# Kernel tuning notes

Measured on AMD Instinct MI355X. Metric: run time of the kernel, lower is better.

## Reference

```python
import jax, jax.numpy as jnp
import numpy as np

N = 50000

def gcn_conv(x, W, b, src, dst, n_nodes):
    # PyG GCNConv: h = x @ W; add self-loops; sym-normalize; scatter-add; + bias
    h = x @ W  # [N, d_out]
    loop = jnp.arange(n_nodes, dtype=src.dtype)
    s = jnp.concatenate([src, loop])
    d = jnp.concatenate([dst, loop])
    deg = jax.ops.segment_sum(jnp.ones_like(d, dtype=h.dtype), d, num_segments=n_nodes)
    dinv = jnp.where(deg > 0, jax.lax.rsqrt(deg), 0.0)
    norm = dinv[s] * dinv[d]  # [E+N]
    msgs = h[s] * norm[:, None]  # gather + scale
    out = jax.ops.segment_sum(msgs, d, num_segments=n_nodes)  # scatter-add
    return out + b

def setup_inputs() -> dict:
    key = jax.random.key(0)
    k1, k2, k3, k4 = jax.random.split(key, 4)
    in_c, hid_c, out_c, E = 512, 256, 64, 800000
    x = jax.random.normal(k1, (N, in_c), dtype=jnp.float32)
    edge_index = jax.random.randint(k2, (2, E), 0, N, dtype=jnp.int64)
    W1 = jax.random.normal(k3, (in_c, hid_c), dtype=jnp.float32) / np.sqrt(in_c)
    b1 = jnp.zeros((hid_c,), dtype=jnp.float32)
    W2 = jax.random.normal(k4, (hid_c, out_c), dtype=jnp.float32) / np.sqrt(hid_c)
    b2 = jnp.zeros((out_c,), dtype=jnp.float32)
    return {"x": x, "edge_index": edge_index, "W1": W1, "b1": b1, "W2": W2, "b2": b2}

def reference(x, edge_index, W1, b1, W2, b2):
    src, dst = edge_index[0], edge_index[1]
    h = gcn_conv(x, W1, b1, src, dst, N)
    h = jax.nn.relu(h)
    h = gcn_conv(h, W2, b2, src, dst, N)
    return jax.nn.log_softmax(h, axis=1)
```

## Files before the change

kernel.cpp:

```cpp
#include <hip/hip_runtime.h>
#include <hip/hip_bf16.h>

#define IN_C 512
#define HID_C 256
#define OUT_C 64

typedef __attribute__((ext_vector_type(8))) short bf16x8;
typedef __attribute__((ext_vector_type(4))) float f32x4;
typedef __attribute__((ext_vector_type(2))) float f32x2;

__device__ __forceinline__ ushort f2bf(float f) {
  __hip_bfloat16 h = __float2bfloat16(f);
  union { __hip_bfloat16 h; ushort u; } v; v.h = h; return v.u;
}
__device__ __forceinline__ uint pack2bf(float a, float b) {
  return (uint)f2bf(a) | ((uint)f2bf(b) << 16);
}
__device__ __forceinline__ float u2f(uint u) {
  union { uint i; float f; } v; v.i = u; return v.f;
}
__device__ __forceinline__ void pkacc(f32x2& aLo, f32x2& aHi, uint ux, uint uy) {
  f32x2 lo, hi;
  lo[0] = u2f(ux << 16);         lo[1] = u2f(uy << 16);
  hi[0] = u2f(ux & 0xffff0000u); hi[1] = u2f(uy & 0xffff0000u);
  aLo += lo;
  aHi += hi;
}
__device__ __forceinline__ void glds16(const ushort* g, ushort* l) {
  __builtin_amdgcn_global_load_lds(
      (const __attribute__((address_space(1))) unsigned int*)(const void*)g,
      (__attribute__((address_space(3))) unsigned int*)(void*)l, 16, 0, 0);
}


__global__ void deg_count(const int* __restrict__ dst, int* __restrict__ counts, int E) {
  int e = blockIdx.x * 256 + threadIdx.x;
  if (e >= E) return;
  atomicAdd(&counts[dst[e]], 1);
}

#define SCAN_TILE 1024

__global__ __launch_bounds__(256) void scan_block_sums(const int* __restrict__ counts,
                                                       int* __restrict__ partial, int n) {
  int base = blockIdx.x * SCAN_TILE + threadIdx.x * 4;
  int s = 0;
  if (base + 3 < n) {
    int4 v = *(const int4*)(counts + base);
    s = v.x + v.y + v.z + v.w;
  } else {
#pragma unroll
    for (int i = 0; i < 4; ++i) if (base + i < n) s += counts[base + i];
  }
#pragma unroll
  for (int off = 1; off < 64; off <<= 1) s += __shfl_xor(s, off);
  __shared__ int ws[4];
  int lane = threadIdx.x & 63, wid = threadIdx.x >> 6;
  if (lane == 0) ws[wid] = s;
  __syncthreads();
  if (threadIdx.x == 0) partial[blockIdx.x] = ws[0] + ws[1] + ws[2] + ws[3];
}

__global__ void scan_partials(int* __restrict__ partial, int nb) {
  int lane = threadIdx.x;
  int carry = 0;
  for (int base = 0; base < nb; base += 64) {
    int i = base + lane;
    int v = (i < nb) ? partial[i] : 0;
    int incl = v;
#pragma unroll
    for (int off = 1; off < 64; off <<= 1) {
      int y = __shfl_up(incl, off);
      if (lane >= off) incl += y;
    }
    if (i < nb) partial[i] = carry + incl - v;
    carry += __shfl(incl, 63);
  }
}

__global__ __launch_bounds__(256) void scan_write(const int* __restrict__ counts,
                                                  const int* __restrict__ partial,
                                                  int* __restrict__ offs,
                                                  int* __restrict__ cur,
                                                  float* __restrict__ dinv,
                                                  int n, int E) {
  int tid = threadIdx.x;
  int base = blockIdx.x * SCAN_TILE + tid * 4;
  int4 c = make_int4(0, 0, 0, 0);
  if (base + 3 < n) {
    c = *(const int4*)(counts + base);
  } else {
    if (base + 0 < n) c.x = counts[base + 0];
    if (base + 1 < n) c.y = counts[base + 1];
    if (base + 2 < n) c.z = counts[base + 2];
  }
  int tsum = c.x + c.y + c.z + c.w;
  int lane = tid & 63, wid = tid >> 6;
  int incl = tsum;
#pragma unroll
  for (int off = 1; off < 64; off <<= 1) {
    int y = __shfl_up(incl, off);
    if (lane >= off) incl += y;
  }
  __shared__ int ws[4];
  if (lane == 63) ws[wid] = incl;
  __syncthreads();
  int wbase = 0;
#pragma unroll
  for (int w = 0; w < 4; ++w) if (w < wid) wbase += ws[w];
  int off0 = partial[blockIdx.x] + wbase + (incl - tsum);
  int4 ov;
  ov.x = off0;
  ov.y = off0 + c.x;
  ov.z = off0 + c.x + c.y;
  ov.w = off0 + c.x + c.y + c.z;
  float4 dv;
  dv.x = rsqrtf((float)(c.x + 1));
  dv.y = rsqrtf((float)(c.y + 1));
  dv.z = rsqrtf((float)(c.z + 1));
  dv.w = rsqrtf((float)(c.w + 1));
  if (base + 3 < n) {
    *(int4*)(offs + base) = ov;
    *(int4*)(cur + base) = ov;
    *(float4*)(dinv + base) = dv;
  } else {
    int o4[4] = {ov.x, ov.y, ov.z, ov.w};
    float d4[4] = {dv.x, dv.y, dv.z, dv.w};
    for (int i = 0; i < 4; ++i)
      if (base + i < n) { offs[base + i] = o4[i]; cur[base + i] = o4[i]; dinv[base + i] = d4[i]; }
  }
  if (blockIdx.x == 0 && tid == 0) offs[n] = E;
}

__global__ void fill_adj(const int* __restrict__ src, const int* __restrict__ dst,
                         int* __restrict__ cur, int* __restrict__ adj, int E) {
  int e = blockIdx.x * 256 + threadIdx.x;
  if (e >= E) return;
  int pos = atomicAdd(&cur[dst[e]], 1);
  adj[pos] = src[e];
}

__global__ __launch_bounds__(256) void transpose_w2(const float* __restrict__ W1,
                                                    ushort* __restrict__ W1t,
                                                    const float* __restrict__ W2,
                                                    ushort* __restrict__ W2t) {
  const float* W; ushort* Wt; int K, N;
  if (blockIdx.z == 0) { W = W1; Wt = W1t; K = IN_C; N = HID_C; }
  else                 { W = W2; Wt = W2t; K = HID_C; N = OUT_C; }
  int n0 = blockIdx.x * 32;
  int k0 = blockIdx.y * 32;
  if (n0 >= N || k0 >= K) return;
  __shared__ ushort t[32][33];
  int tx = threadIdx.x & 31;
  int ty = threadIdx.x >> 5;
#pragma unroll
  for (int i = 0; i < 4; ++i) {
    int k = k0 + ty + i * 8;
    t[ty + i * 8][tx] = f2bf(W[(size_t)k * N + n0 + tx]);
  }
  __syncthreads();
#pragma unroll
  for (int i = 0; i < 4; ++i) {
    int n = n0 + ty + i * 8;
    Wt[(size_t)n * K + k0 + tx] = t[tx][ty + i * 8];
  }
}


__global__ __launch_bounds__(512) void gemm1_fs(const float* __restrict__ A,
                                                const ushort* __restrict__ Bt,
                                                const float* __restrict__ dinv,
                                                ushort* __restrict__ C, int M) {
  __shared__ __align__(16) ushort As[2][128 * 32];
  __shared__ __align__(16) ushort Bs[2][256 * 32];
  int tid = threadIdx.x;
  int lane = tid & 63, wid = tid >> 6;
  int m0 = blockIdx.x * 128;
  int arow = tid >> 2, acol = (tid & 3) * 8;
  int gma = m0 + arow; if (gma >= M) gma = M - 1;
  const float* gA = A + (size_t)gma * IN_C + acol;
  int rb0 = tid >> 2, cb0 = (tid & 3) * 8;
  int rb1 = (tid + 512) >> 2;
  const ushort* gB0 = Bt + (size_t)rb0 * IN_C + cb0;
  const ushort* gB1 = Bt + (size_t)rb1 * IN_C + cb0;

  int wr = wid >> 2, wc = wid & 3;
  int kf = (lane >> 4) * 8, rl = lane & 15;
  f32x4 acc[4][4] = {};

  {
    float4 p0 = *(const float4*)gA;
    float4 p1 = *(const float4*)(gA + 4);
    glds16(gB0, &Bs[0][tid * 8]);
    glds16(gB1, &Bs[0][(tid + 512) * 8]);
    uint4 w;
    w.x = pack2bf(p0.x, p0.y); w.y = pack2bf(p0.z, p0.w);
    w.z = pack2bf(p1.x, p1.y); w.w = pack2bf(p1.z, p1.w);
    *(uint4*)&As[0][arow * 32 + acol] = w;
  }
  __syncthreads();

  int cur = 0;
  for (int t = 0; t < 16; ++t) {
    float4 p0, p1;
    if (t < 15) {
      const float* g = gA + (t + 1) * 32;
      p0 = *(const float4*)g;
      p1 = *(const float4*)(g + 4);
      glds16(gB0 + (t + 1) * 32, &Bs[cur ^ 1][tid * 8]);
      glds16(gB1 + (t + 1) * 32, &Bs[cur ^ 1][(tid + 512) * 8]);
    }
    bf16x8 af[4], bf[4];
#pragma unroll
    for (int i = 0; i < 4; ++i)
      af[i] = *(const bf16x8*)&As[cur][(wr * 64 + i * 16 + rl) * 32 + kf];
#pragma unroll
    for (int j = 0; j < 4; ++j)
      bf[j] = *(const bf16x8*)&Bs[cur][(wc * 64 + j * 16 + rl) * 32 + kf];
#pragma unroll
    for (int i = 0; i < 4; ++i)
#pragma unroll
      for (int j = 0; j < 4; ++j)
        acc[i][j] = __builtin_amdgcn_mfma_f32_16x16x32_bf16(af[i], bf[j], acc[i][j], 0, 0, 0);
    if (t < 15) {
      uint4 w;
      w.x = pack2bf(p0.x, p0.y); w.y = pack2bf(p0.z, p0.w);
      w.z = pack2bf(p1.x, p1.y); w.w = pack2bf(p1.z, p1.w);
      *(uint4*)&As[cur ^ 1][arow * 32 + acol] = w;
    }
    __syncthreads();
    cur ^= 1;
  }

  int r4 = (lane >> 4) * 4;
  int cl = lane & 15;
#pragma unroll
  for (int i = 0; i < 4; ++i) {
#pragma unroll
    for (int r = 0; r < 4; ++r) {
      int gr = m0 + wr * 64 + i * 16 + r4 + r;
      if (gr < M) {
        float dv = dinv[gr];
#pragma unroll
        for (int j = 0; j < 4; ++j) {
          int gc = wc * 64 + j * 16 + cl;
          C[(size_t)gr * HID_C + gc] = f2bf(dv * acc[i][j][r]);
        }
      }
    }
  }
}

__global__ __launch_bounds__(256) void gemm2(const ushort* __restrict__ A,
                                             const ushort* __restrict__ Bt,
                                             const float* __restrict__ dinv,
                                             ushort* __restrict__ C, int M) {
  __shared__ __align__(16) ushort As[2][64 * 32];
  __shared__ __align__(16) ushort Bs[2][64 * 32];
  int tid = threadIdx.x;
  int lane = tid & 63, wid = tid >> 6;
  int m0 = blockIdx.x * 64;
  int arow = tid >> 2, acol = (tid & 3) * 8;
  int gma = m0 + arow; if (gma >= M) gma = M - 1;
  const ushort* gA = A + (size_t)gma * HID_C + acol;
  const ushort* gB = Bt + (size_t)arow * HID_C + acol;

  int wm = wid * 16;
  int kf = (lane >> 4) * 8, rl = lane & 15;
  f32x4 acc[4] = {};

  glds16(gA, &As[0][tid * 8]);
  glds16(gB, &Bs[0][tid * 8]);
  __syncthreads();

  int cur = 0;
  for (int t = 0; t < 8; ++t) {
    if (t < 7) {
      int k0 = (t + 1) * 32;
      glds16(gA + k0, &As[cur ^ 1][tid * 8]);
      glds16(gB + k0, &Bs[cur ^ 1][tid * 8]);
    }
    bf16x8 a, b[4];
    a = *(const bf16x8*)&As[cur][(wm + rl) * 32 + kf];
#pragma unroll
    for (int j = 0; j < 4; ++j)
      b[j] = *(const bf16x8*)&Bs[cur][(j * 16 + rl) * 32 + kf];
#pragma unroll
    for (int j = 0; j < 4; ++j)
      acc[j] = __builtin_amdgcn_mfma_f32_16x16x32_bf16(a, b[j], acc[j], 0, 0, 0);
    __syncthreads();
    cur ^= 1;
  }

  int r4 = (lane >> 4) * 4;
  int cl = lane & 15;
#pragma unroll
  for (int r = 0; r < 4; ++r) {
    int gr = m0 + wm + r4 + r;
    if (gr < M) {
      float dv = dinv[gr];
#pragma unroll
      for (int j = 0; j < 4; ++j) {
        int gc = j * 16 + cl;
        C[(size_t)gr * OUT_C + gc] = f2bf(dv * acc[j][r]);
      }
    }
  }
}


__global__ __launch_bounds__(256) void agg1(const ushort* __restrict__ h,
                                            ushort* __restrict__ out,
                                            const float* __restrict__ dinv,
                                            const int* __restrict__ offs,
                                            const int* __restrict__ adj,
                                            const float* __restrict__ bias, int Nn) {
  int node = blockIdx.x * 4 + (threadIdx.x >> 6);
  if (node >= Nn) return;
  int lane = threadIdx.x & 63;
  int slot = lane >> 4;
  int c0 = (lane & 15) * 16;
  int e0 = offs[node];
  int cnt = offs[node + 1] - e0 + 1;
  const ushort* hc = h + c0;
  f32x2 aLo[4] = {}, aHi[4] = {};
  for (int b0 = 0; b0 < cnt; b0 += 64) {
    int vk = b0 + lane;
    int myadj = node;
    if (vk > 0 && vk < cnt) myadj = adj[e0 + vk - 1];
    int bn = cnt - b0; if (bn > 64) bn = 64;
    int iters = (bn + 3) >> 2;
#pragma unroll 4
    for (int i = 0; i < iters; ++i) {
      int k = slot + 4 * i;
      int s = __shfl(myadj, k < bn ? k : 0);
      if (k < bn) {
        const uint4* rp = (const uint4*)(hc + (size_t)s * HID_C);
        uint4 u0 = rp[0];
        uint4 u1 = rp[1];
        pkacc(aLo[0], aHi[0], u0.x, u0.y);
        pkacc(aLo[1], aHi[1], u0.z, u0.w);
        pkacc(aLo[2], aHi[2], u1.x, u1.y);
        pkacc(aLo[3], aHi[3], u1.z, u1.w);
      }
    }
  }
  float r16[16];
#pragma unroll
  for (int q = 0; q < 4; ++q) {
    r16[4 * q + 0] = aLo[q][0];
    r16[4 * q + 1] = aHi[q][0];
    r16[4 * q + 2] = aLo[q][1];
    r16[4 * q + 3] = aHi[q][1];
  }
#pragma unroll
  for (int i = 0; i < 16; ++i) {
    r16[i] += __shfl_xor(r16[i], 16);
    r16[i] += __shfl_xor(r16[i], 32);
  }
  if (lane < 16) {
    float dv = dinv[node];
    const float4* bp = (const float4*)(bias + c0);
    float bb[16];
#pragma unroll
    for (int q = 0; q < 4; ++q) {
      float4 b4 = bp[q];
      bb[q * 4 + 0] = b4.x; bb[q * 4 + 1] = b4.y;
      bb[q * 4 + 2] = b4.z; bb[q * 4 + 3] = b4.w;
    }
    uint r[8];
#pragma unroll
    for (int i = 0; i < 8; ++i) {
      float v0 = fmaxf(dv * r16[2 * i]     + bb[2 * i],     0.f);
      float v1 = fmaxf(dv * r16[2 * i + 1] + bb[2 * i + 1], 0.f);
      r[i] = (uint)f2bf(v0) | ((uint)f2bf(v1) << 16);
    }
    uint4* op = (uint4*)(out + (size_t)node * HID_C + c0);
    op[0] = make_uint4(r[0], r[1], r[2], r[3]);
    op[1] = make_uint4(r[4], r[5], r[6], r[7]);
  }
}

__global__ __launch_bounds__(256) void agg2(const ushort* __restrict__ h,
                                            float* __restrict__ out,
                                            const float* __restrict__ dinv,
                                            const int* __restrict__ offs,
                                            const int* __restrict__ adj,
                                            const float* __restrict__ bias, int Nn) {
  int node = blockIdx.x * 4 + (threadIdx.x >> 6);
  if (node >= Nn) return;
  int lane = threadIdx.x & 63;
  int slot = lane >> 3;
  int c0 = (lane & 7) * 8;
  int e0 = offs[node];
  int cnt = offs[node + 1] - e0 + 1;
  const ushort* hc = h + c0;
  f32x2 aLo[2] = {}, aHi[2] = {};
  for (int b0 = 0; b0 < cnt; b0 += 64) {
    int vk = b0 + lane;
    int myadj = node;
    if (vk > 0 && vk < cnt) myadj = adj[e0 + vk - 1];
    int bn = cnt - b0; if (bn > 64) bn = 64;
    int iters = (bn + 7) >> 3;
#pragma unroll 4
    for (int i = 0; i < iters; ++i) {
      int k = slot + 8 * i;
      int s = __shfl(myadj, k < bn ? k : 0);
      if (k < bn) {
        uint4 u = *(const uint4*)(hc + (size_t)s * OUT_C);
        pkacc(aLo[0], aHi[0], u.x, u.y);
        pkacc(aLo[1], aHi[1], u.z, u.w);
      }
    }
  }
  float r8[8];
#pragma unroll
  for (int q = 0; q < 2; ++q) {
    r8[4 * q + 0] = aLo[q][0];
    r8[4 * q + 1] = aHi[q][0];
    r8[4 * q + 2] = aLo[q][1];
    r8[4 * q + 3] = aHi[q][1];
  }
#pragma unroll
  for (int i = 0; i < 8; ++i) {
    r8[i] += __shfl_xor(r8[i], 8);
    r8[i] += __shfl_xor(r8[i], 16);
    r8[i] += __shfl_xor(r8[i], 32);
  }
  float dv = dinv[node];
  const float4* bp = (const float4*)(bias + c0);
  float4 bb0 = bp[0], bb1 = bp[1];
  float v[8];
  v[0] = dv * r8[0] + bb0.x; v[1] = dv * r8[1] + bb0.y;
  v[2] = dv * r8[2] + bb0.z; v[3] = dv * r8[3] + bb0.w;
  v[4] = dv * r8[4] + bb1.x; v[5] = dv * r8[5] + bb1.y;
  v[6] = dv * r8[6] + bb1.z; v[7] = dv * r8[7] + bb1.w;
  float m = v[0];
#pragma unroll
  for (int i = 1; i < 8; ++i) m = fmaxf(m, v[i]);
  m = fmaxf(m, __shfl_xor(m, 1));
  m = fmaxf(m, __shfl_xor(m, 2));
  m = fmaxf(m, __shfl_xor(m, 4));
  float s8 = 0.f;
#pragma unroll
  for (int i = 0; i < 8; ++i) s8 += expf(v[i] - m);
  s8 += __shfl_xor(s8, 1);
  s8 += __shfl_xor(s8, 2);
  s8 += __shfl_xor(s8, 4);
  float lg = logf(s8);
  if (lane < 8) {
    float4* op = (float4*)(out + (size_t)node * OUT_C + c0);
    op[0] = make_float4(v[0] - m - lg, v[1] - m - lg, v[2] - m - lg, v[3] - m - lg);
    op[1] = make_float4(v[4] - m - lg, v[5] - m - lg, v[6] - m - lg, v[7] - m - lg);
  }
}


extern "C" void kernel_launch(void* const* d_in, const int* in_sizes, int n_in,
                              void* d_out, int out_size, void* d_ws, size_t ws_size,
                              hipStream_t stream) {
  const float* x  = (const float*)d_in[0];
  const int*   ei = (const int*)d_in[1];
  const float* W1 = (const float*)d_in[2];
  const float* b1 = (const float*)d_in[3];
  const float* W2 = (const float*)d_in[4];
  const float* b2 = (const float*)d_in[5];
  float* outp = (float*)d_out;

  int Nn = in_sizes[0] / IN_C;
  int E  = in_sizes[1] / 2;
  const int* srcv = ei;
  const int* dstv = ei + E;

  char* ws = (char*)d_ws;
  size_t o = 0;
  auto alloc = [&](size_t bytes) {
    char* p = ws + o;
    o = (o + bytes + 255) & ~(size_t)255;
    return p;
  };
  float*  dinv  = (float*)alloc((size_t)Nn * 4);
  int*    counts= (int*)alloc((size_t)Nn * 4);
  int*    offs  = (int*)alloc((size_t)(Nn + 1) * 4);
  int*    cur   = (int*)alloc((size_t)Nn * 4);
  int*    adj   = (int*)alloc((size_t)E * 4);
  int*    partial=(int*)alloc((size_t)((Nn + SCAN_TILE - 1) / SCAN_TILE) * 4);
  ushort* W1t   = (ushort*)alloc((size_t)IN_C * HID_C * 2);
  ushort* W2t   = (ushort*)alloc((size_t)HID_C * OUT_C * 2);
  ushort* h1p   = (ushort*)alloc((size_t)Nn * HID_C * 2);
  ushort* h1a   = (ushort*)alloc((size_t)Nn * HID_C * 2);
  ushort* h2p   = (ushort*)alloc((size_t)Nn * OUT_C * 2);

  int eb = (E + 255) / 256;
  int sb = (Nn + SCAN_TILE - 1) / SCAN_TILE;

  hipMemsetAsync(counts, 0, (size_t)Nn * 4, stream);
  deg_count<<<eb, 256, 0, stream>>>(dstv, counts, E);
  scan_block_sums<<<sb, 256, 0, stream>>>(counts, partial, Nn);
  scan_partials<<<1, 64, 0, stream>>>(partial, sb);
  scan_write<<<sb, 256, 0, stream>>>(counts, partial, offs, cur, dinv, Nn, E);
  fill_adj<<<eb, 256, 0, stream>>>(srcv, dstv, cur, adj, E);
  transpose_w2<<<dim3(HID_C / 32, IN_C / 32, 2), 256, 0, stream>>>(W1, W1t, W2, W2t);

  gemm1_fs<<<(Nn + 127) / 128, 512, 0, stream>>>(x, W1t, dinv, h1p, Nn);
  agg1<<<(Nn + 3) / 4, 256, 0, stream>>>(h1p, h1a, dinv, offs, adj, b1, Nn);
  gemm2<<<(Nn + 63) / 64, 256, 0, stream>>>(h1a, W2t, dinv, h2p, Nn);
  agg2<<<(Nn + 3) / 4, 256, 0, stream>>>(h2p, outp, dinv, offs, adj, b2, Nn);
}
```

Measured before the change: 231.2 us.

## Fuse weight transpose into degree count, inline partial scan, split GEMM1 over N

Merges the weight transpose into the degree-count launch as extra blocks, and drops the single-block partial-scan kernel by having each scan_write block reduce the preceding block partials itself. This removes two kernel launches and one serial tiny kernel. GEMM1 is retiled from 512-thread blocks covering all 256 output columns to 256-thread blocks covering 128 columns, with a second grid dimension. That doubles the block count, but each x row tile is now read and converted twice. The inline scan assumes no more than 64 scan tiles.

```diff
diff --git a/kernel.cpp b/kernel.cpp
--- a/kernel.cpp
+++ b/kernel.cpp
@@ -33,10 +33,37 @@
 }
 
 
-__global__ void deg_count(const int* __restrict__ dst, int* __restrict__ counts, int E) {
-  int e = blockIdx.x * 256 + threadIdx.x;
-  if (e >= E) return;
-  atomicAdd(&counts[dst[e]], 1);
+__global__ void deg_count_tw(const int* __restrict__ dst, int* __restrict__ counts, int E, int eb,
+                             const float* __restrict__ W1, ushort* __restrict__ W1t,
+                             const float* __restrict__ W2, ushort* __restrict__ W2t) {
+  if ((int)blockIdx.x < eb) {
+    int e = blockIdx.x * 256 + threadIdx.x;
+    if (e < E) atomicAdd(&counts[dst[e]], 1);
+    return;
+  }
+  int b2 = blockIdx.x - eb;
+  int z = b2 >> 7;
+  int rem = b2 & 127;
+  int bx = rem & 7, by = rem >> 3;
+  const float* W; ushort* Wt; int K, N;
+  if (z == 0) { W = W1; Wt = W1t; K = IN_C; N = HID_C; }
+  else        { W = W2; Wt = W2t; K = HID_C; N = OUT_C; }
+  int n0 = bx * 32, k0 = by * 32;
+  if (n0 >= N || k0 >= K) return;
+  __shared__ ushort t[32][33];
+  int tx = threadIdx.x & 31;
+  int ty = threadIdx.x >> 5;
+#pragma unroll
+  for (int i = 0; i < 4; ++i) {
+    int k = k0 + ty + i * 8;
+    t[ty + i * 8][tx] = f2bf(W[(size_t)k * N + n0 + tx]);
+  }
+  __syncthreads();
+#pragma unroll
+  for (int i = 0; i < 4; ++i) {
+    int n = n0 + ty + i * 8;
+    Wt[(size_t)n * K + k0 + tx] = t[tx][ty + i * 8];
+  }
 }
 
 #define SCAN_TILE 1024
@@ -61,30 +88,22 @@
   if (threadIdx.x == 0) partial[blockIdx.x] = ws[0] + ws[1] + ws[2] + ws[3];
 }
 
-__global__ void scan_partials(int* __restrict__ partial, int nb) {
-  int lane = threadIdx.x;
-  int carry = 0;
-  for (int base = 0; base < nb; base += 64) {
-    int i = base + lane;
-    int v = (i < nb) ? partial[i] : 0;
-    int incl = v;
-#pragma unroll
-    for (int off = 1; off < 64; off <<= 1) {
-      int y = __shfl_up(incl, off);
-      if (lane >= off) incl += y;
-    }
-    if (i < nb) partial[i] = carry + incl - v;
-    carry += __shfl(incl, 63);
-  }
-}
-
 __global__ __launch_bounds__(256) void scan_write(const int* __restrict__ counts,
                                                   const int* __restrict__ partial,
                                                   int* __restrict__ offs,
                                                   int* __restrict__ cur,
                                                   float* __restrict__ dinv,
-                                                  int n, int E) {
+                                                  int n, int E, int nb) {
+  __shared__ int sbase;
   int tid = threadIdx.x;
+  if (tid < 64) {
+    int v = (tid < (int)blockIdx.x && tid < nb) ? partial[tid] : 0;
+#pragma unroll
+    for (int off = 1; off < 64; off <<= 1) v += __shfl_xor(v, off);
+    if (tid == 0) sbase = v;
+  }
+  __syncthreads();
+  int pbase = sbase;
   int base = blockIdx.x * SCAN_TILE + tid * 4;
   int4 c = make_int4(0, 0, 0, 0);
   if (base + 3 < n) {
@@ -108,7 +127,7 @@
   int wbase = 0;
 #pragma unroll
   for (int w = 0; w < 4; ++w) if (w < wid) wbase += ws[w];
-  int off0 = partial[blockIdx.x] + wbase + (incl - tsum);
+  int off0 = pbase + wbase + (incl - tsum);
   int4 ov;
   ov.x = off0;
   ov.y = off0 + c.x;
@@ -140,93 +159,77 @@
   adj[pos] = src[e];
 }
 
-__global__ __launch_bounds__(256) void transpose_w2(const float* __restrict__ W1,
-                                                    ushort* __restrict__ W1t,
-                                                    const float* __restrict__ W2,
-                                                    ushort* __restrict__ W2t) {
-  const float* W; ushort* Wt; int K, N;
-  if (blockIdx.z == 0) { W = W1; Wt = W1t; K = IN_C; N = HID_C; }
-  else                 { W = W2; Wt = W2t; K = HID_C; N = OUT_C; }
-  int n0 = blockIdx.x * 32;
-  int k0 = blockIdx.y * 32;
-  if (n0 >= N || k0 >= K) return;
-  __shared__ ushort t[32][33];
-  int tx = threadIdx.x & 31;
-  int ty = threadIdx.x >> 5;
-#pragma unroll
-  for (int i = 0; i < 4; ++i) {
-    int k = k0 + ty + i * 8;
-    t[ty + i * 8][tx] = f2bf(W[(size_t)k * N + n0 + tx]);
-  }
-  __syncthreads();
-#pragma unroll
-  for (int i = 0; i < 4; ++i) {
-    int n = n0 + ty + i * 8;
-    Wt[(size_t)n * K + k0 + tx] = t[tx][ty + i * 8];
-  }
-}
-
-
-__global__ __launch_bounds__(512) void gemm1_fs(const float* __restrict__ A,
+
+__global__ __launch_bounds__(256) void gemm1_rs(const float* __restrict__ A,
                                                 const ushort* __restrict__ Bt,
                                                 const float* __restrict__ dinv,
                                                 ushort* __restrict__ C, int M) {
   __shared__ __align__(16) ushort As[2][128 * 32];
-  __shared__ __align__(16) ushort Bs[2][256 * 32];
+  __shared__ __align__(16) ushort Bs[2][128 * 32];
   int tid = threadIdx.x;
   int lane = tid & 63, wid = tid >> 6;
   int m0 = blockIdx.x * 128;
-  int arow = tid >> 2, acol = (tid & 3) * 8;
+  int n0 = blockIdx.y * 128;
+  int arow = tid >> 1, acol = (tid & 1) * 16;
   int gma = m0 + arow; if (gma >= M) gma = M - 1;
   const float* gA = A + (size_t)gma * IN_C + acol;
-  int rb0 = tid >> 2, cb0 = (tid & 3) * 8;
-  int rb1 = (tid + 512) >> 2;
-  const ushort* gB0 = Bt + (size_t)rb0 * IN_C + cb0;
-  const ushort* gB1 = Bt + (size_t)rb1 * IN_C + cb0;
-
-  int wr = wid >> 2, wc = wid & 3;
+  int bcol = (tid & 3) * 8;
+  const ushort* gB0 = Bt + (size_t)(n0 + (tid >> 2)) * IN_C + bcol;
+  const ushort* gB1 = Bt + (size_t)(n0 + ((tid + 256) >> 2)) * IN_C + bcol;
+
+  int wr = wid >> 1, wc = wid & 1;
   int kf = (lane >> 4) * 8, rl = lane & 15;
   f32x4 acc[4][4] = {};
 
   {
-    float4 p0 = *(const float4*)gA;
-    float4 p1 = *(const float4*)(gA + 4);
+    float4 p0 = ((const float4*)gA)[0];
+    float4 p1 = ((const float4*)gA)[1];
+    float4 p2 = ((const float4*)gA)[2];
+    float4 p3 = ((const float4*)gA)[3];
     glds16(gB0, &Bs[0][tid * 8]);
-    glds16(gB1, &Bs[0][(tid + 512) * 8]);
-    uint4 w;
-    w.x = pack2bf(p0.x, p0.y); w.y = pack2bf(p0.z, p0.w);
-    w.z = pack2bf(p1.x, p1.y); w.w = pack2bf(p1.z, p1.w);
-    *(uint4*)&As[0][arow * 32 + acol] = w;
+    glds16(gB1, &Bs[0][(tid + 256) * 8]);
+    uint4 w0, w1;
+    w0.x = pack2bf(p0.x, p0.y); w0.y = pack2bf(p0.z, p0.w);
+    w0.z = pack2bf(p1.x, p1.y); w0.w = pack2bf(p1.z, p1.w);
+    w1.x = pack2bf(p2.x, p2.y); w1.y = pack2bf(p2.z, p2.w);
+    w1.z = pack2bf(p3.x, p3.y); w1.w = pack2bf(p3.z, p3.w);
+    *(uint4*)&As[0][arow * 32 + acol] = w0;
+    *(uint4*)&As[0][arow * 32 + acol + 8] = w1;
   }
   __syncthreads();
 
   int cur = 0;
   for (int t = 0; t < 16; ++t) {
-    float4 p0, p1;
+    float4 p0, p1, p2, p3;
     if (t < 15) {
       const float* g = gA + (t + 1) * 32;
-      p0 = *(const float4*)g;
-      p1 = *(const float4*)(g + 4);
+      p0 = ((const float4*)g)[0];
+      p1 = ((const float4*)g)[1];
+      p2 = ((const float4*)g)[2];
+      p3 = ((const float4*)g)[3];
       glds16(gB0 + (t + 1) * 32, &Bs[cur ^ 1][tid * 8]);
-      glds16(gB1 + (t + 1) * 32, &Bs[cur ^ 1][(tid + 512) * 8]);
-    }
-    bf16x8 af[4], bf[4];
+      glds16(gB1 + (t + 1) * 32, &Bs[cur ^ 1][(tid + 256) * 8]);
+    }
+    bf16x8 af[4], bfr[4];
 #pragma unroll
     for (int i = 0; i < 4; ++i)
       af[i] = *(const bf16x8*)&As[cur][(wr * 64 + i * 16 + rl) * 32 + kf];
 #pragma unroll
     for (int j = 0; j < 4; ++j)
-      bf[j] = *(const bf16x8*)&Bs[cur][(wc * 64 + j * 16 + rl) * 32 + kf];
+      bfr[j] = *(const bf16x8*)&Bs[cur][(wc * 64 + j * 16 + rl) * 32 + kf];
 #pragma unroll
     for (int i = 0; i < 4; ++i)
 #pragma unroll
       for (int j = 0; j < 4; ++j)
-        acc[i][j] = __builtin_amdgcn_mfma_f32_16x16x32_bf16(af[i], bf[j], acc[i][j], 0, 0, 0);
+        acc[i][j] = __builtin_amdgcn_mfma_f32_16x16x32_bf16(af[i], bfr[j], acc[i][j], 0, 0, 0);
     if (t < 15) {
-      uint4 w;
-      w.x = pack2bf(p0.x, p0.y); w.y = pack2bf(p0.z, p0.w);
-      w.z = pack2bf(p1.x, p1.y); w.w = pack2bf(p1.z, p1.w);
-      *(uint4*)&As[cur ^ 1][arow * 32 + acol] = w;
+      uint4 w0, w1;
+      w0.x = pack2bf(p0.x, p0.y); w0.y = pack2bf(p0.z, p0.w);
+      w0.z = pack2bf(p1.x, p1.y); w0.w = pack2bf(p1.z, p1.w);
+      w1.x = pack2bf(p2.x, p2.y); w1.y = pack2bf(p2.z, p2.w);
+      w1.z = pack2bf(p3.x, p3.y); w1.w = pack2bf(p3.z, p3.w);
+      *(uint4*)&As[cur ^ 1][arow * 32 + acol] = w0;
+      *(uint4*)&As[cur ^ 1][arow * 32 + acol + 8] = w1;
     }
     __syncthreads();
     cur ^= 1;
@@ -243,7 +246,7 @@
         float dv = dinv[gr];
 #pragma unroll
         for (int j = 0; j < 4; ++j) {
-          int gc = wc * 64 + j * 16 + cl;
+          int gc = n0 + wc * 64 + j * 16 + cl;
           C[(size_t)gr * HID_C + gc] = f2bf(dv * acc[i][j][r]);
         }
       }
@@ -495,14 +498,12 @@
   int sb = (Nn + SCAN_TILE - 1) / SCAN_TILE;
 
   hipMemsetAsync(counts, 0, (size_t)Nn * 4, stream);
-  deg_count<<<eb, 256, 0, stream>>>(dstv, counts, E);
+  deg_count_tw<<<eb + 256, 256, 0, stream>>>(dstv, counts, E, eb, W1, W1t, W2, W2t);
   scan_block_sums<<<sb, 256, 0, stream>>>(counts, partial, Nn);
-  scan_partials<<<1, 64, 0, stream>>>(partial, sb);
-  scan_write<<<sb, 256, 0, stream>>>(counts, partial, offs, cur, dinv, Nn, E);
+  scan_write<<<sb, 256, 0, stream>>>(counts, partial, offs, cur, dinv, Nn, E, sb);
   fill_adj<<<eb, 256, 0, stream>>>(srcv, dstv, cur, adj, E);
-  transpose_w2<<<dim3(HID_C / 32, IN_C / 32, 2), 256, 0, stream>>>(W1, W1t, W2, W2t);
-
-  gemm1_fs<<<(Nn + 127) / 128, 512, 0, stream>>>(x, W1t, dinv, h1p, Nn);
+
+  gemm1_rs<<<dim3((Nn + 127) / 128, 2), 256, 0, stream>>>(x, W1t, dinv, h1p, Nn);
   agg1<<<(Nn + 3) / 4, 256, 0, stream>>>(h1p, h1a, dinv, offs, adj, b1, Nn);
   gemm2<<<(Nn + 63) / 64, 256, 0, stream>>>(h1a, W2t, dinv, h2p, Nn);
   agg2<<<(Nn + 3) / 4, 256, 0, stream>>>(h2p, outp, dinv, offs, adj, b2, Nn);
```

Measured after the change: 245.9 us. 1.06x slower.
